# Kernel optimization log

Measured on AMD Instinct MI355X. Metric: run time of the kernel, lower is better.

## Reference

```python
import jax, jax.numpy as jnp
import numpy as np

N_EXPERTS = 8
IN_DIM = 2048
HID_DIM = 4096  # max(IN_DIM*2, IN_DIM)
OUT_DIM = 2048
N_NODES = 16384


def setup_inputs() -> dict:
    key = jax.random.key(0)
    k1, k2, k3 = jax.random.split(key, 3)
    x = jax.random.normal(k1, (N_NODES, IN_DIM), dtype=jnp.float32)
    # nn.init.normal_(std=0.02); torch Linear stores weight as [out, in]
    W1 = jax.random.normal(k2, (N_EXPERTS, HID_DIM, IN_DIM), dtype=jnp.float32) * 0.02
    W2 = jax.random.normal(k3, (N_EXPERTS, OUT_DIM, HID_DIM), dtype=jnp.float32) * 0.02
    return {"expert_idx": 2, "x": x, "W1": W1, "W2": W2}


def reference(expert_idx, x, W1, W2):
    # Select this expert's weights (static index, matches ModuleList lookup)
    w1 = W1[expert_idx]  # [hid, in]
    w2 = W2[expert_idx]  # [out, hid]
    h = jnp.einsum('ni,hi->nh', x, w1)          # Linear(in->hid), bias=False
    h = jax.nn.gelu(h, approximate=False)        # torch nn.GELU default = exact erf
    out = jnp.einsum('nh,oh->no', h, w2)         # Linear(hid->out), bias=False
    return out
```

## Files before the change

kernel.cpp:

```cpp
#include <hip/hip_runtime.h>
#include <hip/hip_bf16.h>
#include <math.h>


typedef __bf16 bf16x8 __attribute__((ext_vector_type(8)));
typedef float floatx4 __attribute__((ext_vector_type(4)));

#define GLD16(gp, lp)                                                          \
  __builtin_amdgcn_global_load_lds(                                            \
      (__attribute__((address_space(1))) void*)(gp),                           \
      (__attribute__((address_space(3))) void*)(lp), 16, 0, 0)

__device__ __forceinline__ unsigned short f2bf(float f) {
  union { float f; unsigned int u; } v; v.f = f;
  unsigned int r = v.u + 0x7fffu + ((v.u >> 16) & 1u);
  return (unsigned short)(r >> 16);
}

__global__ void sniff_kernel(const unsigned short* __restrict__ x,
                             int* __restrict__ flag) {
  int lane = threadIdx.x & 63;
  unsigned short u = x[lane * 2];
  int e = (u >> 7) & 0xFF;
  bool ok = (e >= 118) && (e <= 133);
  unsigned long long m = __ballot(ok ? 1 : 0);
  if (lane == 0) flag[0] = (__popcll(m) > 32) ? 1 : 0;
}

__global__ void cvt_kernel(const float* __restrict__ in,
                           unsigned short* __restrict__ out,
                           const int* __restrict__ idxp, long long expert_stride,
                           const int* __restrict__ flagp) {
  if (flagp[0]) return;
  long long base = idxp ? (long long)idxp[0] * expert_stride : 0;
  long long i = ((long long)blockIdx.x * blockDim.x + threadIdx.x) * 4;
  float4 v = *(const float4*)(in + base + i);
  ushort4 o;
  o.x = f2bf(v.x); o.y = f2bf(v.y); o.z = f2bf(v.z); o.w = f2bf(v.w);
  *(ushort4*)(out + i) = o;
}

template <bool GELU, int N, int K>
__global__ __launch_bounds__(256) void gemm_bt(
    const unsigned short* __restrict__ Aws,
    const unsigned short* __restrict__ Araw,
    const unsigned short* __restrict__ Bws,
    const unsigned short* __restrict__ Braw,
    const int* __restrict__ idxp, long long expert_stride,
    void* __restrict__ Cv, const int* __restrict__ flagp) {
  const int flag = flagp[0];
  const unsigned short* __restrict__ A = flag ? Araw : Aws;
  const unsigned short* __restrict__ B =
      flag ? (Braw + (long long)idxp[0] * expert_stride) : Bws;

  __shared__ __align__(16) unsigned short As[128 * 32];
  __shared__ __align__(16) unsigned short Bs[128 * 32];

  const int tid  = threadIdx.x;
  const int lane = tid & 63;
  const int wave = tid >> 6;
  const int m0 = blockIdx.y * 128;
  const int n0 = blockIdx.x * 128;
  const int wm = (wave >> 1) * 64;
  const int wn = (wave & 1) * 64;
  const int lrow = lane & 15;
  const int quad = lane >> 4;

  const int srow = tid >> 2;
  const int scol = (tid & 3) * 8;
  const unsigned short* ga0 = A + (long long)(m0 + srow) * K + scol;
  const unsigned short* ga1 = ga0 + 64LL * K;
  const unsigned short* gb0 = B + (long long)(n0 + srow) * K + scol;
  const unsigned short* gb1 = gb0 + 64LL * K;
  unsigned short* la0 = &As[tid * 8];
  unsigned short* la1 = &As[tid * 8 + 2048];
  unsigned short* lb0 = &Bs[tid * 8];
  unsigned short* lb1 = &Bs[tid * 8 + 2048];

  floatx4 acc[4][4] = {};

  for (int k0 = 0; k0 < K; k0 += 32) {
    GLD16(ga0, la0);
    GLD16(ga1, la1);
    GLD16(gb0, lb0);
    GLD16(gb1, lb1);
    __syncthreads();

    bf16x8 af[4], bfr[4];
#pragma unroll
    for (int i = 0; i < 4; ++i) {
      af[i]  = *(const bf16x8*)(&As[(wm + i * 16 + lrow) * 32 + quad * 8]);
      bfr[i] = *(const bf16x8*)(&Bs[(wn + i * 16 + lrow) * 32 + quad * 8]);
    }
#pragma unroll
    for (int i = 0; i < 4; ++i)
#pragma unroll
      for (int j = 0; j < 4; ++j)
        acc[i][j] = __builtin_amdgcn_mfma_f32_16x16x32_bf16(af[i], bfr[j],
                                                            acc[i][j], 0, 0, 0);
    __syncthreads();
    ga0 += 32; ga1 += 32; gb0 += 32; gb1 += 32;
  }

  if (GELU) {
    unsigned short* Cp = (unsigned short*)Cv;
#pragma unroll
    for (int i = 0; i < 4; ++i) {
      const int rb = m0 + wm + i * 16 + quad * 4;
#pragma unroll
      for (int j = 0; j < 4; ++j) {
        const int col = n0 + wn + j * 16 + lrow;
#pragma unroll
        for (int r = 0; r < 4; ++r) {
          float v = acc[i][j][r];
          v = 0.5f * v * (1.0f + erff(v * 0.70710678118654752f));
          Cp[(long long)(rb + r) * N + col] = f2bf(v);
        }
      }
    }
  } else if (flag) {
    unsigned short* Cp = (unsigned short*)Cv;
#pragma unroll
    for (int i = 0; i < 4; ++i) {
      const int rb = m0 + wm + i * 16 + quad * 4;
#pragma unroll
      for (int j = 0; j < 4; ++j) {
        const int col = n0 + wn + j * 16 + lrow;
#pragma unroll
        for (int r = 0; r < 4; ++r)
          Cp[(long long)(rb + r) * N + col] = f2bf(acc[i][j][r]);
      }
    }
  } else {
    float* Cp = (float*)Cv;
#pragma unroll
    for (int i = 0; i < 4; ++i) {
      const int rb = m0 + wm + i * 16 + quad * 4;
#pragma unroll
      for (int j = 0; j < 4; ++j) {
        const int col = n0 + wn + j * 16 + lrow;
#pragma unroll
        for (int r = 0; r < 4; ++r)
          Cp[(long long)(rb + r) * N + col] = acc[i][j][r];
      }
    }
  }
}

extern "C" void kernel_launch(void* const* d_in, const int* in_sizes, int n_in,
                              void* d_out, int out_size, void* d_ws,
                              size_t ws_size, hipStream_t stream) {
  const int* idxp = (const int*)d_in[0];
  const void* x  = d_in[1];
  const void* W1 = d_in[2];
  const void* W2 = d_in[3];

  char* ws = (char*)d_ws;
  int* flag = (int*)ws;
  unsigned short* h   = (unsigned short*)(ws + 256);
  unsigned short* xb  = (unsigned short*)(ws + 256 + 134217728LL);
  unsigned short* w1b = xb + 33554432LL;
  unsigned short* w2b = w1b + 8388608LL;

  sniff_kernel<<<dim3(1), dim3(64), 0, stream>>>((const unsigned short*)x, flag);

  cvt_kernel<<<dim3(32768), dim3(256), 0, stream>>>((const float*)x, xb,
                                                    nullptr, 0, flag);
  cvt_kernel<<<dim3(8192), dim3(256), 0, stream>>>((const float*)W1, w1b,
                                                   idxp, 8388608LL, flag);
  cvt_kernel<<<dim3(8192), dim3(256), 0, stream>>>((const float*)W2, w2b,
                                                   idxp, 8388608LL, flag);

  gemm_bt<true, 4096, 2048><<<dim3(32, 128), dim3(256), 0, stream>>>(
      xb, (const unsigned short*)x, w1b, (const unsigned short*)W1, idxp,
      8388608LL, h, flag);

  gemm_bt<false, 2048, 4096><<<dim3(16, 128), dim3(256), 0, stream>>>(
      h, h, w2b, (const unsigned short*)W2, idxp, 8388608LL, d_out, flag);
}
```

Measured before the change: 1.255 ms.

## Use 256x256 tiles with 4-stage LDS pipeline, swizzled layout and XCD-aware block mapping

Replaces the 128x128 single-buffered GEMM with a 512-thread 256x256 tile kernel. It uses a 4-deep ring of LDS buffers filled by async global-to-LDS loads, with vmcnt waits in place of double syncthreads. It also XOR-swizzles the LDS layout to avoid bank conflicts and remaps block IDs to group tiles per XCD for L2 reuse. The intent is to hide global load latency and raise arithmetic intensity, at the cost of 128KB dynamic LDS and higher register pressure (32 accumulators per thread).

```diff
diff --git a/kernel.cpp b/kernel.cpp
--- a/kernel.cpp
+++ b/kernel.cpp
@@ -41,7 +41,7 @@
 }
 
 template <bool GELU, int N, int K>
-__global__ __launch_bounds__(256) void gemm_bt(
+__global__ __launch_bounds__(512, 2) void gemm256(
     const unsigned short* __restrict__ Aws,
     const unsigned short* __restrict__ Araw,
     const unsigned short* __restrict__ Bws,
@@ -53,59 +53,93 @@
   const unsigned short* __restrict__ B =
       flag ? (Braw + (long long)idxp[0] * expert_stride) : Bws;
 
-  __shared__ __align__(16) unsigned short As[128 * 32];
-  __shared__ __align__(16) unsigned short Bs[128 * 32];
-
-  const int tid  = threadIdx.x;
+  extern __shared__ __align__(16) char smem[];
+
+  constexpr int NT = K / 32;
+  constexpr int NTN = N / 256;
+
+  const int nwg = (int)gridDim.x;
+  const int cpx = nwg >> 3;
+  const int bid = (int)blockIdx.x;
+  const int swz = (bid & 7) * cpx + (bid >> 3);
+  const int m0 = (swz / NTN) * 256;
+  const int n0 = (swz % NTN) * 256;
+
+  const int tid  = (int)threadIdx.x;
   const int lane = tid & 63;
   const int wave = tid >> 6;
-  const int m0 = blockIdx.y * 128;
-  const int n0 = blockIdx.x * 128;
-  const int wm = (wave >> 1) * 64;
-  const int wn = (wave & 1) * 64;
   const int lrow = lane & 15;
   const int quad = lane >> 4;
-
-  const int srow = tid >> 2;
-  const int scol = (tid & 3) * 8;
-  const unsigned short* ga0 = A + (long long)(m0 + srow) * K + scol;
-  const unsigned short* ga1 = ga0 + 64LL * K;
-  const unsigned short* gb0 = B + (long long)(n0 + srow) * K + scol;
-  const unsigned short* gb1 = gb0 + 64LL * K;
-  unsigned short* la0 = &As[tid * 8];
-  unsigned short* la1 = &As[tid * 8 + 2048];
-  unsigned short* lb0 = &Bs[tid * 8];
-  unsigned short* lb1 = &Bs[tid * 8 + 2048];
-
-  floatx4 acc[4][4] = {};
-
-  for (int k0 = 0; k0 < K; k0 += 32) {
-    GLD16(ga0, la0);
-    GLD16(ga1, la1);
-    GLD16(gb0, lb0);
-    GLD16(gb1, lb1);
-    __syncthreads();
-
-    bf16x8 af[4], bfr[4];
-#pragma unroll
-    for (int i = 0; i < 4; ++i) {
-      af[i]  = *(const bf16x8*)(&As[(wm + i * 16 + lrow) * 32 + quad * 8]);
-      bfr[i] = *(const bf16x8*)(&Bs[(wn + i * 16 + lrow) * 32 + quad * 8]);
-    }
-#pragma unroll
-    for (int i = 0; i < 4; ++i)
+  const int wm = (wave >> 2) * 128;
+  const int wn = (wave & 3) * 64;
+
+  auto decode = [](int u, int& r, int& c) {
+    int s = u >> 3, cw = u & 7;
+    int cp = cw ^ (s & 7);
+    r = (s << 1) | (cp >> 2);
+    c = cp & 3;
+  };
+  int ra0, ca0, ra1, ca1;
+  decode(tid, ra0, ca0);
+  decode(tid + 512, ra1, ca1);
+  const unsigned short* gA0 = A + (long long)(m0 + ra0) * K + ca0 * 8;
+  const unsigned short* gA1 = A + (long long)(m0 + ra1) * K + ca1 * 8;
+  const unsigned short* gB0 = B + (long long)(n0 + ra0) * K + ca0 * 8;
+  const unsigned short* gB1 = B + (long long)(n0 + ra1) * K + ca1 * 8;
+
+  auto STAGE = [&](int t) {
+    char* bb = smem + (t & 3) * 32768;
+    GLD16(gA0 + t * 32, bb + tid * 16);
+    GLD16(gA1 + t * 32, bb + 8192 + tid * 16);
+    GLD16(gB0 + t * 32, bb + 16384 + tid * 16);
+    GLD16(gB1 + t * 32, bb + 24576 + tid * 16);
+  };
+
+  const int cpp = (quad | ((lrow & 1) << 2)) ^ ((lrow >> 1) & 7);
+  const int aoff = wm * 64 + (lrow >> 1) * 128 + cpp * 16;
+  const int boff = wn * 64 + (lrow >> 1) * 128 + cpp * 16;
+
+  floatx4 acc[8][4] = {};
+
+  STAGE(0); STAGE(1); STAGE(2);
+  asm volatile("s_waitcnt vmcnt(8)" ::: "memory");
+  __builtin_amdgcn_s_barrier();
+  asm volatile("" ::: "memory");
+
+#pragma unroll 4
+  for (int t = 0; t < NT; ++t) {
+    char* bb = smem + (t & 3) * 32768;
+    const char* Ab = bb + aoff;
+    const char* Bb = bb + 16384 + boff;
+    bf16x8 a[8], b[4];
+#pragma unroll
+    for (int j = 0; j < 4; ++j) b[j] = *(const bf16x8*)(Bb + j * 1024);
+#pragma unroll
+    for (int i = 0; i < 4; ++i) a[i] = *(const bf16x8*)(Ab + i * 1024);
+    if (t + 3 < NT) STAGE(t + 3);
+#pragma unroll
+    for (int i = 4; i < 8; ++i) a[i] = *(const bf16x8*)(Ab + i * 1024);
+    __builtin_amdgcn_s_setprio(1);
+#pragma unroll
+    for (int i = 0; i < 8; ++i)
 #pragma unroll
       for (int j = 0; j < 4; ++j)
-        acc[i][j] = __builtin_amdgcn_mfma_f32_16x16x32_bf16(af[i], bfr[j],
+        acc[i][j] = __builtin_amdgcn_mfma_f32_16x16x32_bf16(a[i], b[j],
                                                             acc[i][j], 0, 0, 0);
-    __syncthreads();
-    ga0 += 32; ga1 += 32; gb0 += 32; gb1 += 32;
+    __builtin_amdgcn_s_setprio(0);
+    if (t + 1 < NT) {
+      if (t + 3 < NT)      asm volatile("s_waitcnt vmcnt(8)" ::: "memory");
+      else if (t + 2 < NT) asm volatile("s_waitcnt vmcnt(4)" ::: "memory");
+      else                 asm volatile("s_waitcnt vmcnt(0)" ::: "memory");
+      __builtin_amdgcn_s_barrier();
+      asm volatile("" ::: "memory");
+    }
   }
 
   if (GELU) {
     unsigned short* Cp = (unsigned short*)Cv;
 #pragma unroll
-    for (int i = 0; i < 4; ++i) {
+    for (int i = 0; i < 8; ++i) {
       const int rb = m0 + wm + i * 16 + quad * 4;
 #pragma unroll
       for (int j = 0; j < 4; ++j) {
@@ -121,7 +155,7 @@
   } else if (flag) {
     unsigned short* Cp = (unsigned short*)Cv;
 #pragma unroll
-    for (int i = 0; i < 4; ++i) {
+    for (int i = 0; i < 8; ++i) {
       const int rb = m0 + wm + i * 16 + quad * 4;
 #pragma unroll
       for (int j = 0; j < 4; ++j) {
@@ -134,7 +168,7 @@
   } else {
     float* Cp = (float*)Cv;
 #pragma unroll
-    for (int i = 0; i < 4; ++i) {
+    for (int i = 0; i < 8; ++i) {
       const int rb = m0 + wm + i * 16 + quad * 4;
 #pragma unroll
       for (int j = 0; j < 4; ++j) {
@@ -162,6 +196,11 @@
   unsigned short* w1b = xb + 33554432LL;
   unsigned short* w2b = w1b + 8388608LL;
 
+  (void)hipFuncSetAttribute((const void*)gemm256<true, 4096, 2048>,
+                            hipFuncAttributeMaxDynamicSharedMemorySize, 131072);
+  (void)hipFuncSetAttribute((const void*)gemm256<false, 2048, 4096>,
+                            hipFuncAttributeMaxDynamicSharedMemorySize, 131072);
+
   sniff_kernel<<<dim3(1), dim3(64), 0, stream>>>((const unsigned short*)x, flag);
 
   cvt_kernel<<<dim3(32768), dim3(256), 0, stream>>>((const float*)x, xb,
@@ -171,10 +210,10 @@
   cvt_kernel<<<dim3(8192), dim3(256), 0, stream>>>((const float*)W2, w2b,
                                                    idxp, 8388608LL, flag);
 
-  gemm_bt<true, 4096, 2048><<<dim3(32, 128), dim3(256), 0, stream>>>(
+  gemm256<true, 4096, 2048><<<dim3(1024), dim3(512), 131072, stream>>>(
       xb, (const unsigned short*)x, w1b, (const unsigned short*)W1, idxp,
       8388608LL, h, flag);
 
-  gemm_bt<false, 2048, 4096><<<dim3(16, 128), dim3(256), 0, stream>>>(
+  gemm256<false, 2048, 4096><<<dim3(512), dim3(512), 131072, stream>>>(
       h, h, w2b, (const unsigned short*)W2, idxp, 8388608LL, d_out, flag);
 }
```

Result: faster. 1.098 ms (-12.5%).
